# Optimization experiments

Hardware: AMD Instinct MI355X
Metric: run time of the kernel (lower is better)

Reference implementation:

```python
import jax, jax.numpy as jnp
import numpy as np

B, N, C = 256, 25, 256          # batch, joints, in_features
H = 256                          # hidden_features (MLP hidden = H // 2 = 128)


def _build_chain_paths(n):
    """Flatten shortest paths of a chain skeleton (parent[i]=i-1) into
    (heads, ends, pair_ids): edge k of path i->j contributes
    src[:, ends[e]] - src[:, heads[e]] accumulated into pair i*n+j."""
    heads, ends, pair = [], [], []
    for i in range(n):
        for j in range(n):
            step = 1 if j >= i else -1
            cur = i
            while cur != j:
                heads.append(cur)
                ends.append(cur + step)
                pair.append(i * n + j)
                cur += step
    return (np.asarray(heads, np.int32), np.asarray(ends, np.int32),
            np.asarray(pair, np.int32))


def setup_inputs() -> dict:
    key = jax.random.key(0)
    k_src, k_w1, k_w2 = jax.random.split(key, 3)
    heads, ends, pair_ids = _build_chain_paths(N)  # E = 5200 for N=25
    src = jax.random.normal(k_src, (B, N, C), dtype=jnp.float32)
    # torch Linear weights: [out, in], no bias for both edgefeat linears
    W1 = jax.random.normal(k_w1, (H // 2, C), dtype=jnp.float32) / np.sqrt(C)
    W2 = jax.random.normal(k_w2, (1, H // 2), dtype=jnp.float32) / np.sqrt(H // 2)
    alpha = jnp.full((1,), 0.25, dtype=jnp.float32)  # PReLU init
    return {"src": src, "heads": jnp.asarray(heads), "ends": jnp.asarray(ends),
            "pair_ids": jnp.asarray(pair_ids), "W1": W1, "alpha": alpha, "W2": W2}


def reference(src, heads, ends, pair_ids, W1, alpha, W2):
    b, n, c = src.shape
    # gather-subtract along every path edge: [B, E, C]
    diff = src[:, ends, :] - src[:, heads, :]
    # accumulate per (i, j) pair: segment_sum over leading axis -> [N*N, B, C]
    acc = jax.ops.segment_sum(jnp.transpose(diff, (1, 0, 2)), pair_ids,
                              num_segments=n * n)
    edge_feat = jnp.transpose(acc.reshape(n, n, b, c), (2, 0, 1, 3))  # [B,N,N,C]
    h = jnp.einsum('bijc,hc->bijh', edge_feat, W1)   # [B,N,N,H//2]
    h = jnp.where(h >= 0, h, alpha * h)              # PReLU (single shared alpha)
    return jnp.einsum('bijh,oh->bijo', h, W2)        # [B,N,N,1]
```

## Files before the change

### kernel.cpp

```cpp
#include <hip/hip_runtime.h>

#define NJ   25
#define CIN  256
#define HH   128
#define US   136

typedef _Float16 h2  __attribute__((ext_vector_type(2)));
typedef _Float16 h8f __attribute__((ext_vector_type(8)));
typedef __attribute__((ext_vector_type(4))) float f32x4;

__device__ __forceinline__ unsigned short f2h_bits(float f) {
    union { _Float16 h; unsigned short u; } v; v.h = (_Float16)f; return v.u;
}
__device__ __forceinline__ unsigned pack2h(float a, float b) {
    return (unsigned)f2h_bits(a) | ((unsigned)f2h_bits(b) << 16);
}
__device__ __forceinline__ h2 as_h2(unsigned u) {
    union { unsigned u; h2 h; } v; v.u = u; return v.h;
}

__global__ __launch_bounds__(256) void prep_frags(
    const float* __restrict__ src, const float* __restrict__ W1,
    const float* __restrict__ W2,
    unsigned short* __restrict__ srcfrag, unsigned short* __restrict__ w1frag,
    unsigned* __restrict__ w2pk, int nsrc)
{
    const int gid = blockIdx.x * 256 + threadIdx.x;
    const float* base;
    unsigned short* dst;
    if (gid < nsrc) {
        const int lane = gid & 63, kt = (gid >> 6) & 7, mt = (gid >> 9) & 1, b = gid >> 10;
        const int row = mt * 16 + (lane & 15);
        const int k0  = kt * 32 + (lane >> 4) * 8;
        dst = srcfrag + (size_t)gid * 8;
        if (row >= NJ) { *(uint4*)dst = make_uint4(0u, 0u, 0u, 0u); return; }
        base = src + ((size_t)b * NJ + row) * CIN + k0;
    } else if (gid < nsrc + 4096) {
        const int id = gid - nsrc;
        const int lane = id & 63, kt = (id >> 6) & 7, nt = id >> 9;
        const int row = nt * 16 + (lane & 15);
        const int k0  = kt * 32 + (lane >> 4) * 8;
        dst = w1frag + (size_t)id * 8;
        base = W1 + (size_t)row * CIN + k0;
    } else {
        const int id = gid - nsrc - 4096;
        if (id < HH / 2) w2pk[id] = pack2h(W2[2 * id], W2[2 * id + 1]);
        return;
    }
    float4 x = *(const float4*)base;
    float4 y = *(const float4*)(base + 4);
    uint4 o;
    o.x = pack2h(x.x, x.y); o.y = pack2h(x.z, x.w);
    o.z = pack2h(y.x, y.y); o.w = pack2h(y.z, y.w);
    *(uint4*)dst = o;
}

__global__ __launch_bounds__(512) void fused_edge_mlp_v6(
    const unsigned short* __restrict__ srcfrag,
    const unsigned short* __restrict__ w1frag,
    const unsigned* __restrict__ w2pk,
    const float* __restrict__ Aarr,
    float* __restrict__ out)
{
    __shared__ unsigned short u16[NJ * US];
    __shared__ float s_s[NJ];

    const int b    = blockIdx.x;
    const int t    = threadIdx.x;
    const int w    = t >> 6;
    const int lane = t & 63;
    const int ln15 = lane & 15;
    const int quad = lane >> 4;
    const int hcol = w * 16 + ln15;

    {
        const h8f* w1p = (const h8f*)w1frag + (w * 8) * 64 + lane;
        const h8f* ap  = (const h8f*)srcfrag + ((size_t)b * 16) * 64 + lane;

        h8f bfrag[8];
        #pragma unroll
        for (int kt = 0; kt < 8; ++kt) bfrag[kt] = w1p[kt * 64];

        f32x4 acc0 = {0.f, 0.f, 0.f, 0.f};
        f32x4 acc1 = {0.f, 0.f, 0.f, 0.f};
        #pragma unroll
        for (int kt = 0; kt < 8; ++kt) {
            acc0 = __builtin_amdgcn_mfma_f32_16x16x32_f16(ap[kt * 64],       bfrag[kt], acc0, 0, 0, 0);
            acc1 = __builtin_amdgcn_mfma_f32_16x16x32_f16(ap[(8 + kt) * 64], bfrag[kt], acc1, 0, 0, 0);
        }

        #pragma unroll
        for (int r = 0; r < 4; ++r) {
            int m0 = quad * 4 + r;
            if (m0 < NJ) u16[m0 * US + hcol] = f2h_bits(acc0[r]);
            int m1 = 16 + quad * 4 + r;
            if (m1 < NJ) u16[m1 * US + hcol] = f2h_bits(acc1[r]);
        }
    }
    __syncthreads();

    const float alpha = Aarr[0];
    float* outb = out + (size_t)b * (NJ * NJ);
    const uint4* w2v = (const uint4*)w2pk;

    float M = 0.f;
    int i = 0, j = 0;
    if (t < 300) {
        i = (int)((49.0f - sqrtf(2401.0f - 8.0f * (float)t)) * 0.5f);
        {
            int Si = (49 * i - i * i) >> 1;
            if (t < Si) { --i; }
            else { int Sn = (49 * (i + 1) - (i + 1) * (i + 1)) >> 1; if (t >= Sn) ++i; }
        }
        const int S = (49 * i - i * i) >> 1;
        j = t - S + i + 1;

        const uint4* ujp = (const uint4*)(u16 + j * US);
        const uint4* uip = (const uint4*)(u16 + i * US);
        #pragma unroll
        for (int h8 = 0; h8 < 16; ++h8) {
            uint4 a = ujp[h8], c = uip[h8], ww = w2v[h8];
            h2 mx;
            mx = __builtin_elementwise_max(as_h2(a.x), as_h2(c.x));
            M  = __builtin_amdgcn_fdot2(mx, as_h2(ww.x), M, false);
            mx = __builtin_elementwise_max(as_h2(a.y), as_h2(c.y));
            M  = __builtin_amdgcn_fdot2(mx, as_h2(ww.y), M, false);
            mx = __builtin_elementwise_max(as_h2(a.z), as_h2(c.z));
            M  = __builtin_amdgcn_fdot2(mx, as_h2(ww.z), M, false);
            mx = __builtin_elementwise_max(as_h2(a.w), as_h2(c.w));
            M  = __builtin_amdgcn_fdot2(mx, as_h2(ww.w), M, false);
        }
    } else if (t < 300 + NJ) {
        const int r = t - 300;
        const uint4* up = (const uint4*)(u16 + r * US);
        float s = 0.f;
        #pragma unroll
        for (int h8 = 0; h8 < 16; ++h8) {
            uint4 a = up[h8], ww = w2v[h8];
            s = __builtin_amdgcn_fdot2(as_h2(a.x), as_h2(ww.x), s, false);
            s = __builtin_amdgcn_fdot2(as_h2(a.y), as_h2(ww.y), s, false);
            s = __builtin_amdgcn_fdot2(as_h2(a.z), as_h2(ww.z), s, false);
            s = __builtin_amdgcn_fdot2(as_h2(a.w), as_h2(ww.w), s, false);
        }
        s_s[r] = s;
    }
    __syncthreads();

    if (t < 300) {
        const float sj = s_s[j], si = s_s[i];
        const float Mw = (1.f - alpha) * M;
        outb[i * NJ + j] = Mw + alpha * sj - si;
        outb[j * NJ + i] = Mw + alpha * si - sj;
    } else if (t >= 325 && t < 350) {
        const int r = t - 325;
        outb[r * (NJ + 1)] = 0.f;
    }
}

extern "C" void kernel_launch(void* const* d_in, const int* in_sizes, int n_in,
                              void* d_out, int out_size, void* d_ws, size_t ws_size,
                              hipStream_t stream) {
    const float* src   = (const float*)d_in[0];
    const float* W1    = (const float*)d_in[4];
    const float* alpha = (const float*)d_in[5];
    const float* W2    = (const float*)d_in[6];
    float* out = (float*)d_out;

    const int B    = in_sizes[0] / (NJ * CIN);
    const int nsrc = B * 16 * 64;
    unsigned short* srcfrag = (unsigned short*)d_ws;
    unsigned short* w1frag  = srcfrag + (size_t)nsrc * 8;
    unsigned*       w2pk    = (unsigned*)(w1frag + 4096 * 8);

    const int totalA = nsrc + 4096 + HH / 2;
    prep_frags<<<(totalA + 255) / 256, 256, 0, stream>>>(src, W1, W2, srcfrag, w1frag, w2pk, nsrc);
    fused_edge_mlp_v6<<<B, 512, 0, stream>>>(srcfrag, w1frag, w2pk, alpha, out);
}
```

Before: 73.76 us.

## Fuse src fp16 conversion into main kernel via LDS staging

The fp16 packing of src moves out of the prep kernel and into the main kernel. Each block loads its batch's src rows in fp32, converts them to fp16 and stores them in padded LDS, then builds the MFMA A fragments from LDS. This removes the global round trip through the srcfrag workspace and shrinks the prep kernel to the weights only. In exchange it adds an extra barrier, more LDS traffic and larger LDS use per block.

```diff
diff --git a/kernel.cpp b/kernel.cpp
--- a/kernel.cpp
+++ b/kernel.cpp
@@ -3,9 +3,11 @@
 #define NJ   25
 #define CIN  256
 #define HH   128
+#define SS   264
 #define US   136
 
 typedef _Float16 h2  __attribute__((ext_vector_type(2)));
+typedef _Float16 h4  __attribute__((ext_vector_type(4)));
 typedef _Float16 h8f __attribute__((ext_vector_type(8)));
 typedef __attribute__((ext_vector_type(4))) float f32x4;
 
@@ -19,49 +21,36 @@
     union { unsigned u; h2 h; } v; v.u = u; return v.h;
 }
 
-__global__ __launch_bounds__(256) void prep_frags(
-    const float* __restrict__ src, const float* __restrict__ W1,
-    const float* __restrict__ W2,
-    unsigned short* __restrict__ srcfrag, unsigned short* __restrict__ w1frag,
-    unsigned* __restrict__ w2pk, int nsrc)
+__global__ __launch_bounds__(256) void prep_w(
+    const float* __restrict__ W1, const float* __restrict__ W2,
+    unsigned short* __restrict__ w1frag, unsigned* __restrict__ w2pk)
 {
     const int gid = blockIdx.x * 256 + threadIdx.x;
-    const float* base;
-    unsigned short* dst;
-    if (gid < nsrc) {
-        const int lane = gid & 63, kt = (gid >> 6) & 7, mt = (gid >> 9) & 1, b = gid >> 10;
-        const int row = mt * 16 + (lane & 15);
-        const int k0  = kt * 32 + (lane >> 4) * 8;
-        dst = srcfrag + (size_t)gid * 8;
-        if (row >= NJ) { *(uint4*)dst = make_uint4(0u, 0u, 0u, 0u); return; }
-        base = src + ((size_t)b * NJ + row) * CIN + k0;
-    } else if (gid < nsrc + 4096) {
-        const int id = gid - nsrc;
-        const int lane = id & 63, kt = (id >> 6) & 7, nt = id >> 9;
+    if (gid < 4096) {
+        const int lane = gid & 63, kt = (gid >> 6) & 7, nt = gid >> 9;
         const int row = nt * 16 + (lane & 15);
         const int k0  = kt * 32 + (lane >> 4) * 8;
-        dst = w1frag + (size_t)id * 8;
-        base = W1 + (size_t)row * CIN + k0;
-    } else {
-        const int id = gid - nsrc - 4096;
-        if (id < HH / 2) w2pk[id] = pack2h(W2[2 * id], W2[2 * id + 1]);
-        return;
+        const float* base = W1 + (size_t)row * CIN + k0;
+        float4 x = *(const float4*)base;
+        float4 y = *(const float4*)(base + 4);
+        uint4 o;
+        o.x = pack2h(x.x, x.y); o.y = pack2h(x.z, x.w);
+        o.z = pack2h(y.x, y.y); o.w = pack2h(y.z, y.w);
+        *(uint4*)(w1frag + (size_t)gid * 8) = o;
+    } else if (gid < 4096 + HH / 2) {
+        const int id = gid - 4096;
+        w2pk[id] = pack2h(W2[2 * id], W2[2 * id + 1]);
     }
-    float4 x = *(const float4*)base;
-    float4 y = *(const float4*)(base + 4);
-    uint4 o;
-    o.x = pack2h(x.x, x.y); o.y = pack2h(x.z, x.w);
-    o.z = pack2h(y.x, y.y); o.w = pack2h(y.z, y.w);
-    *(uint4*)dst = o;
 }
 
-__global__ __launch_bounds__(512) void fused_edge_mlp_v6(
-    const unsigned short* __restrict__ srcfrag,
+__global__ __launch_bounds__(512) void fused_edge_mlp_v8(
+    const float* __restrict__ src,
     const unsigned short* __restrict__ w1frag,
     const unsigned* __restrict__ w2pk,
     const float* __restrict__ Aarr,
     float* __restrict__ out)
 {
+    __shared__ unsigned short s_lds[NJ * SS];
     __shared__ unsigned short u16[NJ * US];
     __shared__ float s_s[NJ];
 
@@ -74,19 +63,45 @@
     const int hcol = w * 16 + ln15;
 
     {
+        const float4* s4 = (const float4*)(src + (size_t)b * NJ * CIN);
+        for (int idx = t; idx < NJ * CIN / 4; idx += 512) {
+            const int n = idx >> 6, k4 = idx & 63;
+            float4 v = s4[idx];
+            uint2 o = make_uint2(pack2h(v.x, v.y), pack2h(v.z, v.w));
+            *(uint2*)&s_lds[n * SS + k4 * 4] = o;
+        }
+    }
+    __syncthreads();
+
+    {
         const h8f* w1p = (const h8f*)w1frag + (w * 8) * 64 + lane;
-        const h8f* ap  = (const h8f*)srcfrag + ((size_t)b * 16) * 64 + lane;
-
         h8f bfrag[8];
         #pragma unroll
         for (int kt = 0; kt < 8; ++kt) bfrag[kt] = w1p[kt * 64];
+
+        const int r1   = 16 + ln15;
+        const bool r1ok = (r1 < NJ);
+        const int cbase = quad * 8;
 
         f32x4 acc0 = {0.f, 0.f, 0.f, 0.f};
         f32x4 acc1 = {0.f, 0.f, 0.f, 0.f};
         #pragma unroll
         for (int kt = 0; kt < 8; ++kt) {
-            acc0 = __builtin_amdgcn_mfma_f32_16x16x32_f16(ap[kt * 64],       bfrag[kt], acc0, 0, 0, 0);
-            acc1 = __builtin_amdgcn_mfma_f32_16x16x32_f16(ap[(8 + kt) * 64], bfrag[kt], acc1, 0, 0, 0);
+            const int co = kt * 32 + cbase;
+            h4 lo0 = *(const h4*)&s_lds[ln15 * SS + co];
+            h4 hi0 = *(const h4*)&s_lds[ln15 * SS + co + 4];
+            h8f a0;
+            a0[0] = lo0[0]; a0[1] = lo0[1]; a0[2] = lo0[2]; a0[3] = lo0[3];
+            a0[4] = hi0[0]; a0[5] = hi0[1]; a0[6] = hi0[2]; a0[7] = hi0[3];
+            h8f a1 = {};
+            if (r1ok) {
+                h4 lo1 = *(const h4*)&s_lds[r1 * SS + co];
+                h4 hi1 = *(const h4*)&s_lds[r1 * SS + co + 4];
+                a1[0] = lo1[0]; a1[1] = lo1[1]; a1[2] = lo1[2]; a1[3] = lo1[3];
+                a1[4] = hi1[0]; a1[5] = hi1[1]; a1[6] = hi1[2]; a1[7] = hi1[3];
+            }
+            acc0 = __builtin_amdgcn_mfma_f32_16x16x32_f16(a0, bfrag[kt], acc0, 0, 0, 0);
+            acc1 = __builtin_amdgcn_mfma_f32_16x16x32_f16(a1, bfrag[kt], acc1, 0, 0, 0);
         }
 
         #pragma unroll
@@ -166,13 +181,10 @@
     const float* W2    = (const float*)d_in[6];
     float* out = (float*)d_out;
 
-    const int B    = in_sizes[0] / (NJ * CIN);
-    const int nsrc = B * 16 * 64;
-    unsigned short* srcfrag = (unsigned short*)d_ws;
-    unsigned short* w1frag  = srcfrag + (size_t)nsrc * 8;
-    unsigned*       w2pk    = (unsigned*)(w1frag + 4096 * 8);
+    const int B = in_sizes[0] / (NJ * CIN);
+    unsigned short* w1frag = (unsigned short*)d_ws;
+    unsigned*       w2pk   = (unsigned*)(w1frag + 4096 * 8);
 
-    const int totalA = nsrc + 4096 + HH / 2;
-    prep_frags<<<(totalA + 255) / 256, 256, 0, stream>>>(src, W1, W2, srcfrag, w1frag, w2pk, nsrc);
-    fused_edge_mlp_v6<<<B, 512, 0, stream>>>(srcfrag, w1frag, w2pk, alpha, out);
+    prep_w<<<17, 256, 0, stream>>>(W1, W2, w1frag, w2pk);
+    fused_edge_mlp_v8<<<B, 512, 0, stream>>>(src, w1frag, w2pk, alpha, out);
 }
```

Result: no change. 72.49 us (-1.7%).
